# Optimization experiments

Hardware: AMD Instinct MI355X
Metric: run time of the kernel (lower is better)

The kernel has to match this reference:

```python
import jax, jax.numpy as jnp
import numpy as np

N = 100000   # nodes
F = 128      # feature len
E = 1600000  # edges per graph (avg degree 16)


def setup_inputs() -> dict:
    key = jax.random.key(0)
    ks = jax.random.split(key, 32)
    def nrm(k, shape, scale=0.05):
        return jax.random.normal(k, shape, jnp.float32) * scale
    inp = {"X": jax.random.normal(ks[0], (N, F), jnp.float32)}
    i = 1
    for g in (1, 2, 3):
        inp[f"edge_index{g}"] = jax.random.randint(ks[i], (2, E), 0, N, dtype=jnp.int32); i += 1
        inp[f"edge_weight{g}"] = jax.random.uniform(ks[i], (E,), jnp.float32); i += 1
        inp[f"g{g}_w1"] = nrm(ks[i], (F, F)); i += 1
        inp[f"g{g}_b1"] = jnp.zeros((F,), jnp.float32)
        inp[f"g{g}_w2"] = nrm(ks[i], (F, F)); i += 1
        inp[f"g{g}_b2"] = jnp.zeros((F,), jnp.float32)
    for name in ("fc1", "fc2"):
        inp[f"{name}_w1"] = nrm(ks[i], (F, 256)); i += 1
        inp[f"{name}_b1"] = jnp.zeros((256,), jnp.float32)
        inp[f"{name}_w2"] = nrm(ks[i], (256, 128)); i += 1
        inp[f"{name}_b2"] = jnp.zeros((128,), jnp.float32)
        inp[f"{name}_w3"] = nrm(ks[i], (128, 64)); i += 1
        inp[f"{name}_b3"] = jnp.zeros((64,), jnp.float32)
    return inp


def gcn_conv(x, w, b, src, dst, ew):
    # PyG GCNConv: add self-loops (weight 1), symmetric normalization.
    n = x.shape[0]
    h = x @ w                                                   # [N, F]
    deg = jax.ops.segment_sum(ew, dst, num_segments=n) + 1.0    # [N]
    dinv = jax.lax.rsqrt(deg)
    norm = dinv[src] * ew * dinv[dst]                           # [E]
    agg = jax.ops.segment_sum(h[src] * norm[:, None], dst, num_segments=n)
    agg = agg + (dinv * dinv)[:, None] * h                      # self-loop term
    return agg + b


def single_module(x, src, dst, ew, w1, b1, w2, b2):
    x = jax.nn.relu(gcn_conv(x, w1, b1, src, dst, ew))
    x = jax.nn.relu(gcn_conv(x, w2, b2, src, dst, ew))
    return x


def fc_layer(x, w1, b1, w2, b2, w3, b3):
    x = jax.nn.relu(x @ w1 + b1)
    x = jax.nn.relu(x @ w2 + b2)
    return jax.nn.relu(x @ w3 + b3)


def reference(X, edge_index1, edge_weight1, g1_w1, g1_b1, g1_w2, g1_b2,
              edge_index2, edge_weight2, g2_w1, g2_b1, g2_w2, g2_b2,
              edge_index3, edge_weight3, g3_w1, g3_b1, g3_w2, g3_b2,
              fc1_w1, fc1_b1, fc1_w2, fc1_b2, fc1_w3, fc1_b3,
              fc2_w1, fc2_b1, fc2_w2, fc2_b2, fc2_w3, fc2_b3):
    X0 = fc_layer(X, fc1_w1, fc1_b1, fc1_w2, fc1_b2, fc1_w3, fc1_b3)
    X1 = single_module(X, edge_index1[0], edge_index1[1], edge_weight1, g1_w1, g1_b1, g1_w2, g1_b2)
    X1 = fc_layer(X1, fc2_w1, fc2_b1, fc2_w2, fc2_b2, fc2_w3, fc2_b3)
    X2 = single_module(X, edge_index2[0], edge_index2[1], edge_weight2, g2_w1, g2_b1, g2_w2, g2_b2)
    X2 = fc_layer(X2, fc2_w1, fc2_b1, fc2_w2, fc2_b2, fc2_w3, fc2_b3)
    X3 = single_module(X, edge_index3[0], edge_index3[1], edge_weight3, g3_w1, g3_b1, g3_w2, g3_b2)
    X3 = fc_layer(X3, fc2_w1, fc2_b1, fc2_w2, fc2_b2, fc2_w3, fc2_b3)
    Xs = X0 + X1 + X2 + X3
    return (Xs, X1, X2, X3)
```

## Files before the change

### kernel.cpp

```cpp
#include <hip/hip_runtime.h>


typedef short bf16x8 __attribute__((ext_vector_type(8)));
typedef float f32x4 __attribute__((ext_vector_type(4)));

#define BSHIFT 8
#define NBUCK_MAX 400
#define BCAP 6144
#define WDSCALE 8388608.f

static __device__ __forceinline__ float frelu(float x) { return x > 0.f ? x : 0.f; }

static __device__ __forceinline__ unsigned short f2bf(float f) {
    unsigned int u = __float_as_uint(f);
    u += 0x7fffu + ((u >> 16) & 1u);
    return (unsigned short)(u >> 16);
}
static __device__ __forceinline__ float bflo(unsigned int u) {
    return __uint_as_float(u << 16);
}
static __device__ __forceinline__ float bfhi(unsigned int u) {
    return __uint_as_float(u & 0xffff0000u);
}

__global__ void xconv(const float* __restrict__ src, unsigned short* __restrict__ dst, int n4) {
    int i = blockIdx.x * 256 + threadIdx.x;
    if (i >= n4) return;
    float4 v = *(const float4*)(src + (size_t)i * 4);
    ushort4 o = {f2bf(v.x), f2bf(v.y), f2bf(v.z), f2bf(v.w)};
    *(ushort4*)(dst + (size_t)i * 4) = o;
}

__global__ void wtrans(const float* __restrict__ src, unsigned short* __restrict__ dst,
                       int K, int M) {
    int i = blockIdx.x * 256 + threadIdx.x;
    if (i >= K * M) return;
    int m = i / K, k = i % K;
    dst[i] = f2bf(src[(size_t)k * M + m]);
}

__global__ void zero_small(int* __restrict__ p, int n) {
    int i = blockIdx.x * 256 + threadIdx.x;
    if (i < n) p[i] = 0;
}

__global__ __launch_bounds__(256) void part_k(
    const int* __restrict__ src, const int* __restrict__ dst,
    const float* __restrict__ ew, int* __restrict__ gcur,
    int2* __restrict__ part, int nE, int nbuck) {
    __shared__ int lh[4][NBUCK_MAX];
    __shared__ int gb[4][NBUCK_MAX];
    const int tid = threadIdx.x;
    const int w = tid >> 6;
    for (int t = tid; t < 4 * NBUCK_MAX; t += 256) ((int*)lh)[t] = 0;
    __syncthreads();
    const int e0 = blockIdx.x * 4096;
    int rk[16], bk[16];
#pragma unroll
    for (int j = 0; j < 16; ++j) {
        int e = e0 + j * 256 + tid;
        rk[j] = -1;
        if (e < nE) {
            int b = dst[e] >> BSHIFT;
            bk[j] = b;
            rk[j] = atomicAdd(&lh[w][b], 1);
        }
    }
    __syncthreads();
    for (int t = tid; t < nbuck; t += 256) {
        int c0 = lh[0][t], c1 = lh[1][t], c2 = lh[2][t], c3 = lh[3][t];
        int tot = c0 + c1 + c2 + c3;
        int base = tot ? atomicAdd(&gcur[t], tot) : 0;
        gb[0][t] = base;
        gb[1][t] = base + c0;
        gb[2][t] = base + c0 + c1;
        gb[3][t] = base + c0 + c1 + c2;
    }
    __syncthreads();
#pragma unroll
    for (int j = 0; j < 16; ++j) {
        int e = e0 + j * 256 + tid;
        if (e >= nE) continue;
        int b = bk[j];
        int slot = gb[w][b] + rk[j];
        if (slot >= 0 && slot < BCAP) {
            int s = src[e];
            int dl = dst[e] & ((1 << BSHIFT) - 1);
            part[(size_t)b * BCAP + slot] = make_int2(s | (dl << 17), __float_as_int(ew[e]));
        }
    }
}

__global__ void scanB(const int* __restrict__ gcur, int* __restrict__ bbase,
                      int* __restrict__ rp, int n, int nbuck) {
    __shared__ int s[512];
    int t = threadIdx.x;
    int c = (t < nbuck) ? gcur[t] : 0;
    if (c > BCAP) c = BCAP;
    s[t] = c;
    __syncthreads();
#pragma unroll
    for (int off = 1; off < 512; off <<= 1) {
        int x = (t >= off) ? s[t - off] : 0;
        __syncthreads();
        s[t] += x;
        __syncthreads();
    }
    if (t < nbuck) bbase[t] = s[t] - c;
    if (t == nbuck - 1) rp[n] = s[t];
}

__global__ __launch_bounds__(256) void csr_bucket(
    const int2* __restrict__ part, const int* __restrict__ gcur,
    const int* __restrict__ bbase, int2* __restrict__ ev,
    int* __restrict__ rp, float* __restrict__ dinv, int n) {
    __shared__ int hist[256];
    __shared__ int cur[256];
    __shared__ int wd[256];
    const int b = blockIdx.x;
    const int t = threadIdx.x;
    int cnt = gcur[b];
    if (cnt > BCAP) cnt = BCAP;
    const int gbase = bbase[b];
    const int2* pb = part + (size_t)b * BCAP;

    hist[t] = 0; wd[t] = 0;
    __syncthreads();
    for (int i = t; i < cnt; i += 256)
        atomicAdd(&hist[(pb[i].x >> 17) & 255], 1);
    __syncthreads();
    int myh = hist[t];
#pragma unroll
    for (int off = 1; off < 256; off <<= 1) {
        int x = (t >= off) ? hist[t - off] : 0;
        __syncthreads();
        hist[t] += x;
        __syncthreads();
    }
    int excl = hist[t] - myh;
    cur[t] = excl;
    __syncthreads();
    for (int i = t; i < cnt; i += 256) {
        int2 p = pb[i];
        int dl = (p.x >> 17) & 255;
        int pos = atomicAdd(&cur[dl], 1);
        ev[(size_t)gbase + pos] = make_int2(p.x & 0x1FFFF, p.y);
        atomicAdd(&wd[dl], (int)(__int_as_float(p.y) * WDSCALE + 0.5f));
    }
    __syncthreads();
    int g = (b << BSHIFT) + t;
    if (g < n) {
        dinv[g] = rsqrtf(1.f + (float)wd[t] * (1.f / WDSCALE));
        rp[g] = gbase + excl;
    }
}

__global__ __launch_bounds__(256) void gather_bf(
    const int* __restrict__ rp, const int2* __restrict__ ev,
    const unsigned short* __restrict__ h,
    const float* __restrict__ dinv, const float* __restrict__ bias,
    unsigned short* __restrict__ aggr, int n) {
    int node = (int)(((size_t)blockIdx.x * 256 + threadIdx.x) >> 6);
    if (node >= n) return;
    int lane = threadIdx.x & 63;
    float di = dinv[node];
    float sl = di * di;
    unsigned int hu = *(const unsigned int*)(h + (size_t)node * 128 + lane * 2);
    float2 bv = *(const float2*)(bias + lane * 2);
    float ax0 = 0.f, ay0 = 0.f, ax1 = 0.f, ay1 = 0.f;
    float ax2 = 0.f, ay2 = 0.f, ax3 = 0.f, ay3 = 0.f;
    const int beg = rp[node], end = rp[node + 1];
    int i = beg;
    for (; i + 7 < end; i += 8) {
        int2 e[8];
#pragma unroll
        for (int j = 0; j < 8; ++j) e[j] = ev[i + j];
        float nm[8];
#pragma unroll
        for (int j = 0; j < 8; ++j) nm[j] = dinv[e[j].x] * __int_as_float(e[j].y);
        unsigned int u[8];
#pragma unroll
        for (int j = 0; j < 8; ++j)
            u[j] = *(const unsigned int*)(h + (size_t)e[j].x * 128 + lane * 2);
        ax0 += nm[0] * bflo(u[0]); ay0 += nm[0] * bfhi(u[0]);
        ax1 += nm[1] * bflo(u[1]); ay1 += nm[1] * bfhi(u[1]);
        ax2 += nm[2] * bflo(u[2]); ay2 += nm[2] * bfhi(u[2]);
        ax3 += nm[3] * bflo(u[3]); ay3 += nm[3] * bfhi(u[3]);
        ax0 += nm[4] * bflo(u[4]); ay0 += nm[4] * bfhi(u[4]);
        ax1 += nm[5] * bflo(u[5]); ay1 += nm[5] * bfhi(u[5]);
        ax2 += nm[6] * bflo(u[6]); ay2 += nm[6] * bfhi(u[6]);
        ax3 += nm[7] * bflo(u[7]); ay3 += nm[7] * bfhi(u[7]);
    }
    for (; i + 3 < end; i += 4) {
        int2 e0 = ev[i], e1 = ev[i + 1], e2 = ev[i + 2], e3 = ev[i + 3];
        float n0 = dinv[e0.x] * __int_as_float(e0.y);
        float n1 = dinv[e1.x] * __int_as_float(e1.y);
        float n2 = dinv[e2.x] * __int_as_float(e2.y);
        float n3 = dinv[e3.x] * __int_as_float(e3.y);
        unsigned int u0 = *(const unsigned int*)(h + (size_t)e0.x * 128 + lane * 2);
        unsigned int u1 = *(const unsigned int*)(h + (size_t)e1.x * 128 + lane * 2);
        unsigned int u2 = *(const unsigned int*)(h + (size_t)e2.x * 128 + lane * 2);
        unsigned int u3 = *(const unsigned int*)(h + (size_t)e3.x * 128 + lane * 2);
        ax0 += n0 * bflo(u0); ay0 += n0 * bfhi(u0);
        ax1 += n1 * bflo(u1); ay1 += n1 * bfhi(u1);
        ax2 += n2 * bflo(u2); ay2 += n2 * bfhi(u2);
        ax3 += n3 * bflo(u3); ay3 += n3 * bfhi(u3);
    }
    for (; i < end; ++i) {
        int2 e0 = ev[i];
        float n0 = dinv[e0.x] * __int_as_float(e0.y);
        unsigned int u0 = *(const unsigned int*)(h + (size_t)e0.x * 128 + lane * 2);
        ax0 += n0 * bflo(u0); ay0 += n0 * bfhi(u0);
    }
    float ox = frelu(di * ((ax0 + ax1) + (ax2 + ax3)) + sl * bflo(hu) + bv.x);
    float oy = frelu(di * ((ay0 + ay1) + (ay2 + ay3)) + sl * bfhi(hu) + bv.y);
    unsigned int o = (unsigned int)f2bf(ox) | ((unsigned int)f2bf(oy) << 16);
    *(unsigned int*)(aggr + (size_t)node * 128 + lane * 2) = o;
}

template<int K, int BN, int RELU, int EPI>
__global__ __launch_bounds__(256, 2) void gemm_bf(
    const unsigned short* __restrict__ A, const unsigned short* __restrict__ Wt,
    const float* __restrict__ bias, void* __restrict__ Cout,
    int M, int nrows, float* __restrict__ xs) {
    constexpr int BM = 128, BK = 64;
    constexpr int WN = BN / 2;
    constexpr int NF = WN / 16;
    static_assert(BN == 64 || BN == 128, "BN");
    __shared__ unsigned short As[BM][BK + 8];
    __shared__ unsigned short Bs[BN][BK + 8];

    const int tid  = threadIdx.x;
    const int wid  = tid >> 6;
    const int lane = tid & 63;
    const int wm   = (wid >> 1) * 64;
    const int wn   = (wid & 1) * WN;
    const int row0 = blockIdx.x * BM;
    const int col0 = blockIdx.y * BN;
    const int lr   = lane & 15;
    const int lk   = (lane >> 4) * 8;

    f32x4 acc[4][NF] = {};

    for (int k0 = 0; k0 < K; k0 += BK) {
#pragma unroll
        for (int it = 0; it < 4; ++it) {
            int f = tid + it * 256;
            int r = f >> 3, g = f & 7;
            int grow = row0 + r;
            if (grow >= nrows) grow = nrows - 1;
            bf16x8 v = *(const bf16x8*)(A + (size_t)grow * K + k0 + g * 8);
            *(bf16x8*)&As[r][g * 8] = v;
        }
#pragma unroll
        for (int it = 0; it < BN / 32; ++it) {
            int f = tid + it * 256;
            int nidx = f >> 3, g = f & 7;
            bf16x8 v = *(const bf16x8*)(Wt + (size_t)(col0 + nidx) * K + k0 + g * 8);
            *(bf16x8*)&Bs[nidx][g * 8] = v;
        }
        __syncthreads();
#pragma unroll
        for (int kk = 0; kk < 2; ++kk) {
            bf16x8 af[4], bfv[NF];
#pragma unroll
            for (int mi = 0; mi < 4; ++mi)
                af[mi] = *(const bf16x8*)&As[wm + 16 * mi + lr][kk * 32 + lk];
#pragma unroll
            for (int ni = 0; ni < NF; ++ni)
                bfv[ni] = *(const bf16x8*)&Bs[wn + 16 * ni + lr][kk * 32 + lk];
#pragma unroll
            for (int mi = 0; mi < 4; ++mi)
#pragma unroll
                for (int ni = 0; ni < NF; ++ni)
                    acc[mi][ni] = __builtin_amdgcn_mfma_f32_16x16x32_bf16(
                        af[mi], bfv[ni], acc[mi][ni], 0, 0, 0);
        }
        __syncthreads();
    }

    const int dr0 = (lane >> 4) * 4;
#pragma unroll
    for (int ni = 0; ni < NF; ++ni) {
        int col = col0 + wn + 16 * ni + lr;
        float bv = bias ? bias[col] : 0.f;
#pragma unroll
        for (int mi = 0; mi < 4; ++mi) {
#pragma unroll
            for (int r = 0; r < 4; ++r) {
                int grow = row0 + wm + 16 * mi + dr0 + r;
                if (grow >= nrows) continue;
                float v = acc[mi][ni][r] + bv;
                if (RELU) v = frelu(v);
                if (EPI == 0) {
                    ((unsigned short*)Cout)[(size_t)grow * M + col] = f2bf(v);
                } else {
                    ((float*)Cout)[(size_t)grow * M + col] = v;
                    if (EPI == 2) xs[(size_t)grow * 64 + col] += v;
                }
            }
        }
    }
}

template<int EPI>
__global__ __launch_bounds__(256, 2) void fc_chain(
    const unsigned short* __restrict__ A,
    const unsigned short* __restrict__ W1t, const float* __restrict__ b1,
    const unsigned short* __restrict__ W2t, const float* __restrict__ b2,
    const unsigned short* __restrict__ W3t, const float* __restrict__ b3,
    float* __restrict__ Cout, int nrows, float* __restrict__ xs) {
    __shared__ unsigned short Ain[128 * 136];
    __shared__ unsigned short T1q[128 * 72];
    __shared__ unsigned short Bst[128 * 72];

    const int tid  = threadIdx.x;
    const int wid  = tid >> 6;
    const int lane = tid & 63;
    const int wm   = (wid >> 1) * 64;
    const int wnH  = (wid & 1) * 32;
    const int wnF  = (wid & 1) * 64;
    const int row0 = blockIdx.x * 128;
    const int lr   = lane & 15;
    const int lk   = (lane >> 4) * 8;
    const int dr0  = (lane >> 4) * 4;

#pragma unroll
    for (int it = 0; it < 8; ++it) {
        int f = tid + it * 256;
        int r = f >> 4, g = f & 15;
        int grow = row0 + r; if (grow >= nrows) grow = nrows - 1;
        *(bf16x8*)&Ain[r * 136 + g * 8] =
            *(const bf16x8*)(A + (size_t)grow * 128 + g * 8);
    }

    f32x4 acc2[4][4] = {};

    for (int q = 0; q < 4; ++q) {
        __syncthreads();
#pragma unroll
        for (int it = 0; it < 4; ++it) {
            int f = tid + it * 256;
            int r = f >> 4, g = f & 15;
            *(bf16x8*)&Bst[r * 136 + g * 8] =
                *(const bf16x8*)(W1t + (size_t)(q * 64 + r) * 128 + g * 8);
        }
        __syncthreads();
        f32x4 acc1[4][2] = {};
#pragma unroll
        for (int kk = 0; kk < 4; ++kk) {
            bf16x8 af[4], bw[2];
#pragma unroll
            for (int mi = 0; mi < 4; ++mi)
                af[mi] = *(const bf16x8*)&Ain[(wm + 16 * mi + lr) * 136 + kk * 32 + lk];
#pragma unroll
            for (int ni = 0; ni < 2; ++ni)
                bw[ni] = *(const bf16x8*)&Bst[(wnH + 16 * ni + lr) * 136 + kk * 32 + lk];
#pragma unroll
            for (int mi = 0; mi < 4; ++mi)
#pragma unroll
                for (int ni = 0; ni < 2; ++ni)
                    acc1[mi][ni] = __builtin_amdgcn_mfma_f32_16x16x32_bf16(
                        af[mi], bw[ni], acc1[mi][ni], 0, 0, 0);
        }
        __syncthreads();
#pragma unroll
        for (int ni = 0; ni < 2; ++ni) {
            float bv = b1[q * 64 + wnH + 16 * ni + lr];
#pragma unroll
            for (int mi = 0; mi < 4; ++mi)
#pragma unroll
                for (int r = 0; r < 4; ++r)
                    T1q[(wm + 16 * mi + dr0 + r) * 72 + wnH + 16 * ni + lr] =
                        f2bf(frelu(acc1[mi][ni][r] + bv));
        }
#pragma unroll
        for (int it = 0; it < 4; ++it) {
            int f = tid + it * 256;
            int r = f >> 3, g = f & 7;
            *(bf16x8*)&Bst[r * 72 + g * 8] =
                *(const bf16x8*)(W2t + (size_t)r * 256 + q * 64 + g * 8);
        }
        __syncthreads();
#pragma unroll
        for (int kk = 0; kk < 2; ++kk) {
            bf16x8 af[4], bw[4];
#pragma unroll
            for (int mi = 0; mi < 4; ++mi)
                af[mi] = *(const bf16x8*)&T1q[(wm + 16 * mi + lr) * 72 + kk * 32 + lk];
#pragma unroll
            for (int ni = 0; ni < 4; ++ni)
                bw[ni] = *(const bf16x8*)&Bst[(wnF + 16 * ni + lr) * 72 + kk * 32 + lk];
#pragma unroll
            for (int mi = 0; mi < 4; ++mi)
#pragma unroll
                for (int ni = 0; ni < 4; ++ni)
                    acc2[mi][ni] = __builtin_amdgcn_mfma_f32_16x16x32_bf16(
                        af[mi], bw[ni], acc2[mi][ni], 0, 0, 0);
        }
    }
    __syncthreads();
#pragma unroll
    for (int ni = 0; ni < 4; ++ni) {
        float bv = b2[wnF + 16 * ni + lr];
#pragma unroll
        for (int mi = 0; mi < 4; ++mi)
#pragma unroll
            for (int r = 0; r < 4; ++r)
                Ain[(wm + 16 * mi + dr0 + r) * 136 + wnF + 16 * ni + lr] =
                    f2bf(frelu(acc2[mi][ni][r] + bv));
    }
#pragma unroll
    for (int it = 0; it < 4; ++it) {
        int f = tid + it * 256;
        int r = f >> 4, g = f & 15;
        *(bf16x8*)&Bst[r * 136 + g * 8] =
            *(const bf16x8*)(W3t + (size_t)r * 128 + g * 8);
    }
    __syncthreads();
    f32x4 acc3[4][2] = {};
#pragma unroll
    for (int kk = 0; kk < 4; ++kk) {
        bf16x8 af[4], bw[2];
#pragma unroll
        for (int mi = 0; mi < 4; ++mi)
            af[mi] = *(const bf16x8*)&Ain[(wm + 16 * mi + lr) * 136 + kk * 32 + lk];
#pragma unroll
        for (int ni = 0; ni < 2; ++ni)
            bw[ni] = *(const bf16x8*)&Bst[(wnH + 16 * ni + lr) * 136 + kk * 32 + lk];
#pragma unroll
        for (int mi = 0; mi < 4; ++mi)
#pragma unroll
            for (int ni = 0; ni < 2; ++ni)
                acc3[mi][ni] = __builtin_amdgcn_mfma_f32_16x16x32_bf16(
                    af[mi], bw[ni], acc3[mi][ni], 0, 0, 0);
    }
#pragma unroll
    for (int ni = 0; ni < 2; ++ni) {
        int col = wnH + 16 * ni + lr;
        float bv = b3[col];
#pragma unroll
        for (int mi = 0; mi < 4; ++mi)
#pragma unroll
            for (int r = 0; r < 4; ++r) {
                int grow = row0 + wm + 16 * mi + dr0 + r;
                if (grow >= nrows) continue;
                float v = frelu(acc3[mi][ni][r] + bv);
                Cout[(size_t)grow * 64 + col] = v;
                if (EPI == 2) xs[(size_t)grow * 64 + col] += v;
            }
    }
}

extern "C" void kernel_launch(void* const* d_in, const int* in_sizes, int n_in,
                              void* d_out, int out_size, void* d_ws, size_t ws_size,
                              hipStream_t stream) {
    (void)n_in; (void)out_size; (void)ws_size;
    const float* X = (const float*)d_in[0];
    const int N = in_sizes[0] / 128;

    const float* fc1_w1 = (const float*)d_in[19];
    const float* fc1_b1 = (const float*)d_in[20];
    const float* fc1_w2 = (const float*)d_in[21];
    const float* fc1_b2 = (const float*)d_in[22];
    const float* fc1_w3 = (const float*)d_in[23];
    const float* fc1_b3 = (const float*)d_in[24];
    const float* fc2_w1 = (const float*)d_in[25];
    const float* fc2_b1 = (const float*)d_in[26];
    const float* fc2_w2 = (const float*)d_in[27];
    const float* fc2_b2 = (const float*)d_in[28];
    const float* fc2_w3 = (const float*)d_in[29];
    const float* fc2_b3 = (const float*)d_in[30];

    float* out = (float*)d_out;
    float* Xs  = out;

    char* base = (char*)d_ws;
    const size_t Npad = (((size_t)N + 255) / 256) * 256;
    float*          dinv  = (float*)base;                 base += Npad * 4;
    unsigned short* Xbf   = (unsigned short*)base;        base += (size_t)N * 128 * 2;
    unsigned short* t1bf  = (unsigned short*)base;        base += (size_t)N * 256 * 2;
    unsigned short* t2bf  = (unsigned short*)base;        base += (size_t)N * 128 * 2;
    unsigned short* aggbf = (unsigned short*)base;        base += (size_t)N * 128 * 2;
    unsigned short* wtbuf = (unsigned short*)base;

    unsigned short* fc1w1t = wtbuf;
    unsigned short* fc1w2t = fc1w1t + 32768;
    unsigned short* fc1w3t = fc1w2t + 32768;
    unsigned short* fc2w1t = fc1w3t + 8192;
    unsigned short* fc2w2t = fc2w1t + 32768;
    unsigned short* fc2w3t = fc2w2t + 32768;
    unsigned short* gwt    = fc2w3t + 8192;

    const dim3 blk(256);
    const int GR = (N + 127) / 128;
    const int NBUCK = (N + 255) >> 8;
    const int GWB = (int)(((size_t)N * 64 + 255) / 256);

    xconv<<<(N * 32 + 255) / 256, blk, 0, stream>>>(X, Xbf, N * 32);
    wtrans<<<(128 * 256 + 255) / 256, blk, 0, stream>>>(fc1_w1, fc1w1t, 128, 256);
    wtrans<<<(256 * 128 + 255) / 256, blk, 0, stream>>>(fc1_w2, fc1w2t, 256, 128);
    wtrans<<<(128 * 64 + 255) / 256, blk, 0, stream>>>(fc1_w3, fc1w3t, 128, 64);
    wtrans<<<(128 * 256 + 255) / 256, blk, 0, stream>>>(fc2_w1, fc2w1t, 128, 256);
    wtrans<<<(256 * 128 + 255) / 256, blk, 0, stream>>>(fc2_w2, fc2w2t, 256, 128);
    wtrans<<<(128 * 64 + 255) / 256, blk, 0, stream>>>(fc2_w3, fc2w3t, 128, 64);
    for (int g = 0; g < 3; ++g) {
        wtrans<<<(128 * 128 + 255) / 256, blk, 0, stream>>>(
            (const float*)d_in[3 + 6 * g], gwt + g * 32768, 128, 128);
        wtrans<<<(128 * 128 + 255) / 256, blk, 0, stream>>>(
            (const float*)d_in[5 + 6 * g], gwt + g * 32768 + 16384, 128, 128);
    }

    fc_chain<1><<<GR, blk, 0, stream>>>(Xbf, fc1w1t, fc1_b1, fc1w2t, fc1_b2,
                                        fc1w3t, fc1_b3, Xs, N, nullptr);

    for (int g = 0; g < 3; ++g) {
        const int*   ei  = (const int*)d_in[1 + 6 * g];
        const int    E   = in_sizes[1 + 6 * g] / 2;
        const int*   srp = ei;
        const int*   dsp = ei + E;
        const float* ew  = (const float*)d_in[2 + 6 * g];
        const float* b1  = (const float*)d_in[4 + 6 * g];
        const float* b2  = (const float*)d_in[6 + 6 * g];
        unsigned short* w1t = gwt + g * 32768;
        unsigned short* w2t = w1t + 16384;

        int2* part  = (int2*)t1bf;
        int2* ev    = part + (size_t)NBUCK * BCAP;
        int*  rpn   = (int*)(ev + E);
        int*  gcur  = rpn + (N + 1);
        int*  bbase = gcur + NBUCK;

        zero_small<<<(NBUCK + 255) / 256, blk, 0, stream>>>(gcur, NBUCK);
        part_k<<<(E + 4095) / 4096, blk, 0, stream>>>(srp, dsp, ew, gcur, part, E, NBUCK);
        scanB<<<1, 512, 0, stream>>>(gcur, bbase, rpn, N, NBUCK);
        csr_bucket<<<NBUCK, blk, 0, stream>>>(part, gcur, bbase, ev, rpn, dinv, N);

        gemm_bf<128, 128, 0, 0><<<dim3(GR, 1), blk, 0, stream>>>(Xbf, w1t, nullptr, t2bf, 128, N, nullptr);
        gather_bf<<<GWB, blk, 0, stream>>>(rpn, ev, t2bf, dinv, b1, aggbf, N);
        gemm_bf<128, 128, 0, 0><<<dim3(GR, 1), blk, 0, stream>>>(aggbf, w2t, nullptr, t2bf, 128, N, nullptr);
        gather_bf<<<GWB, blk, 0, stream>>>(rpn, ev, t2bf, dinv, b2, aggbf, N);

        fc_chain<2><<<GR, blk, 0, stream>>>(aggbf, fc2w1t, fc2_b1, fc2w2t, fc2_b2,
                                            fc2w3t, fc2_b3,
                                            out + (size_t)(1 + g) * N * 64, N, Xs);
    }
}
```

Baseline: 970.8 us.

## Batch weight transposes into one launch and sort CSR rows deterministically in LDS

Twelve separate weight-transpose launches are merged into one segmented kernel, and the three per-graph zeroing launches are replaced by a single upfront zero of three counter arrays. This cuts the number of small kernel launches. csr_bucket now stages each bucket in a shared-memory buffer, insertion-sorts every row by source, sums the degree in float instead of with fixed-point atomics, and then writes the edges out coalesced. The sort makes edge order and degree deterministic, but it adds serial per-thread sorting work and a large LDS allocation (48KB) that can reduce occupancy.

```diff
diff --git a/kernel.cpp b/kernel.cpp
--- a/kernel.cpp
+++ b/kernel.cpp
@@ -7,7 +7,6 @@
 #define BSHIFT 8
 #define NBUCK_MAX 400
 #define BCAP 6144
-#define WDSCALE 8388608.f
 
 static __device__ __forceinline__ float frelu(float x) { return x > 0.f ? x : 0.f; }
 
@@ -31,12 +30,25 @@
     *(ushort4*)(dst + (size_t)i * 4) = o;
 }
 
-__global__ void wtrans(const float* __restrict__ src, unsigned short* __restrict__ dst,
-                       int K, int M) {
-    int i = blockIdx.x * 256 + threadIdx.x;
-    if (i >= K * M) return;
-    int m = i / K, k = i % K;
-    dst[i] = f2bf(src[(size_t)k * M + m]);
+struct WSegs {
+    const float* src[13];
+    unsigned short* dst[13];
+    int beg[14];
+    int ksh[13];
+    int M[13];
+};
+
+__global__ void wtrans_all(WSegs segs, int total) {
+    int idx = blockIdx.x * 256 + threadIdx.x;
+    if (idx >= total) return;
+    int s = 0;
+#pragma unroll
+    for (int i = 1; i < 13; ++i) s += (idx >= segs.beg[i]);
+    int li = idx - segs.beg[s];
+    int ksh = segs.ksh[s];
+    int m = li >> ksh;
+    int k = li & ((1 << ksh) - 1);
+    segs.dst[s][li] = f2bf(segs.src[s][(size_t)k * segs.M[s] + m]);
 }
 
 __global__ void zero_small(int* __restrict__ p, int n) {
@@ -116,7 +128,7 @@
     int* __restrict__ rp, float* __restrict__ dinv, int n) {
     __shared__ int hist[256];
     __shared__ int cur[256];
-    __shared__ int wd[256];
+    __shared__ int2 sbuf[BCAP];
     const int b = blockIdx.x;
     const int t = threadIdx.x;
     int cnt = gcur[b];
@@ -124,7 +136,7 @@
     const int gbase = bbase[b];
     const int2* pb = part + (size_t)b * BCAP;
 
-    hist[t] = 0; wd[t] = 0;
+    hist[t] = 0;
     __syncthreads();
     for (int i = t; i < cnt; i += 256)
         atomicAdd(&hist[(pb[i].x >> 17) & 255], 1);
@@ -144,15 +156,27 @@
         int2 p = pb[i];
         int dl = (p.x >> 17) & 255;
         int pos = atomicAdd(&cur[dl], 1);
-        ev[(size_t)gbase + pos] = make_int2(p.x & 0x1FFFF, p.y);
-        atomicAdd(&wd[dl], (int)(__int_as_float(p.y) * WDSCALE + 0.5f));
-    }
-    __syncthreads();
-    int g = (b << BSHIFT) + t;
-    if (g < n) {
-        dinv[g] = rsqrtf(1.f + (float)wd[t] * (1.f / WDSCALE));
-        rp[g] = gbase + excl;
-    }
+        sbuf[pos] = make_int2(p.x & 0x1FFFF, p.y);
+    }
+    __syncthreads();
+    {
+        for (int i = excl + 1; i < excl + myh; ++i) {
+            int2 key = sbuf[i];
+            int j = i - 1;
+            while (j >= excl && sbuf[j].x > key.x) { sbuf[j + 1] = sbuf[j]; --j; }
+            sbuf[j + 1] = key;
+        }
+        float wdeg = 1.f;
+        for (int i = excl; i < excl + myh; ++i) wdeg += __int_as_float(sbuf[i].y);
+        int g = (b << BSHIFT) + t;
+        if (g < n) {
+            dinv[g] = rsqrtf(wdeg);
+            rp[g] = gbase + excl;
+        }
+    }
+    __syncthreads();
+    for (int i = t; i < cnt; i += 256)
+        ev[(size_t)gbase + i] = sbuf[i];
 }
 
 __global__ __launch_bounds__(256) void gather_bf(
@@ -459,17 +483,11 @@
     const float* X = (const float*)d_in[0];
     const int N = in_sizes[0] / 128;
 
-    const float* fc1_w1 = (const float*)d_in[19];
     const float* fc1_b1 = (const float*)d_in[20];
-    const float* fc1_w2 = (const float*)d_in[21];
     const float* fc1_b2 = (const float*)d_in[22];
-    const float* fc1_w3 = (const float*)d_in[23];
     const float* fc1_b3 = (const float*)d_in[24];
-    const float* fc2_w1 = (const float*)d_in[25];
     const float* fc2_b1 = (const float*)d_in[26];
-    const float* fc2_w2 = (const float*)d_in[27];
     const float* fc2_b2 = (const float*)d_in[28];
-    const float* fc2_w3 = (const float*)d_in[29];
     const float* fc2_b3 = (const float*)d_in[30];
 
     float* out = (float*)d_out;
@@ -482,7 +500,9 @@
     unsigned short* t1bf  = (unsigned short*)base;        base += (size_t)N * 256 * 2;
     unsigned short* t2bf  = (unsigned short*)base;        base += (size_t)N * 128 * 2;
     unsigned short* aggbf = (unsigned short*)base;        base += (size_t)N * 128 * 2;
-    unsigned short* wtbuf = (unsigned short*)base;
+    unsigned short* wtbuf = (unsigned short*)base;        base += 245760 * 2;
+    int*            gcur3 = (int*)base;                   base += 3 * NBUCK_MAX * 4;
+    int*            bbase = (int*)base;                   base += NBUCK_MAX * 4;
 
     unsigned short* fc1w1t = wtbuf;
     unsigned short* fc1w2t = fc1w1t + 32768;
@@ -498,18 +518,35 @@
     const int GWB = (int)(((size_t)N * 64 + 255) / 256);
 
     xconv<<<(N * 32 + 255) / 256, blk, 0, stream>>>(X, Xbf, N * 32);
-    wtrans<<<(128 * 256 + 255) / 256, blk, 0, stream>>>(fc1_w1, fc1w1t, 128, 256);
-    wtrans<<<(256 * 128 + 255) / 256, blk, 0, stream>>>(fc1_w2, fc1w2t, 256, 128);
-    wtrans<<<(128 * 64 + 255) / 256, blk, 0, stream>>>(fc1_w3, fc1w3t, 128, 64);
-    wtrans<<<(128 * 256 + 255) / 256, blk, 0, stream>>>(fc2_w1, fc2w1t, 128, 256);
-    wtrans<<<(256 * 128 + 255) / 256, blk, 0, stream>>>(fc2_w2, fc2w2t, 256, 128);
-    wtrans<<<(128 * 64 + 255) / 256, blk, 0, stream>>>(fc2_w3, fc2w3t, 128, 64);
-    for (int g = 0; g < 3; ++g) {
-        wtrans<<<(128 * 128 + 255) / 256, blk, 0, stream>>>(
-            (const float*)d_in[3 + 6 * g], gwt + g * 32768, 128, 128);
-        wtrans<<<(128 * 128 + 255) / 256, blk, 0, stream>>>(
-            (const float*)d_in[5 + 6 * g], gwt + g * 32768 + 16384, 128, 128);
-    }
+    {
+        WSegs segs;
+        const float* srcs[13] = {
+            (const float*)d_in[19], (const float*)d_in[21], (const float*)d_in[23],
+            (const float*)d_in[25], (const float*)d_in[27], (const float*)d_in[29],
+            (const float*)d_in[3],  (const float*)d_in[5],
+            (const float*)d_in[9],  (const float*)d_in[11],
+            (const float*)d_in[15], (const float*)d_in[17]
+        };
+        unsigned short* dsts[13] = {
+            fc1w1t, fc1w2t, fc1w3t, fc2w1t, fc2w2t, fc2w3t,
+            gwt, gwt + 16384, gwt + 32768, gwt + 49152, gwt + 65536, gwt + 81920
+        };
+        int ksh[13] = {7, 8, 7, 7, 8, 7, 7, 7, 7, 7, 7, 7};
+        int Ms[13]  = {256, 128, 64, 256, 128, 64, 128, 128, 128, 128, 128, 128};
+        int sz[13]  = {32768, 32768, 8192, 32768, 32768, 8192,
+                       16384, 16384, 16384, 16384, 16384, 16384};
+        int acc = 0;
+        for (int i = 0; i < 12; ++i) {
+            segs.src[i] = srcs[i]; segs.dst[i] = dsts[i];
+            segs.ksh[i] = ksh[i];  segs.M[i] = Ms[i];
+            segs.beg[i] = acc;     acc += sz[i];
+        }
+        segs.src[12] = srcs[11]; segs.dst[12] = dsts[11];
+        segs.ksh[12] = 7; segs.M[12] = 128;
+        segs.beg[12] = acc; segs.beg[13] = acc;
+        wtrans_all<<<(acc + 255) / 256, blk, 0, stream>>>(segs, acc);
+    }
+    zero_small<<<(3 * NBUCK_MAX + 255) / 256, blk, 0, stream>>>(gcur3, 3 * NBUCK_MAX);
 
     fc_chain<1><<<GR, blk, 0, stream>>>(Xbf, fc1w1t, fc1_b1, fc1w2t, fc1_b2,
                                         fc1w3t, fc1_b3, Xs, N, nullptr);
@@ -522,16 +559,14 @@
         const float* ew  = (const float*)d_in[2 + 6 * g];
         const float* b1  = (const float*)d_in[4 + 6 * g];
         const float* b2  = (const float*)d_in[6 + 6 * g];
-        unsigned short* w1t = gwt + g * 32768;
+        unsigned short* w1t = gwt + (size_t)g * 32768;
         unsigned short* w2t = w1t + 16384;
+        int* gcur = gcur3 + g * NBUCK_MAX;
 
         int2* part  = (int2*)t1bf;
         int2* ev    = part + (size_t)NBUCK * BCAP;
         int*  rpn   = (int*)(ev + E);
-        int*  gcur  = rpn + (N + 1);
-        int*  bbase = gcur + NBUCK;
-
-        zero_small<<<(NBUCK + 255) / 256, blk, 0, stream>>>(gcur, NBUCK);
+
         part_k<<<(E + 4095) / 4096, blk, 0, stream>>>(srp, dsp, ew, gcur, part, E, NBUCK);
         scanB<<<1, 512, 0, stream>>>(gcur, bbase, rpn, N, NBUCK);
         csr_bucket<<<NBUCK, blk, 0, stream>>>(part, gcur, bbase, ev, rpn, dinv, N);
```

After: 1.072 ms. 10.4% more time.
